# Kernel tuning notes

Hardware: AMD Instinct MI355X
Metric: run time of the kernel (lower is better)

Reference implementation:

```python
import jax, jax.numpy as jnp
import numpy as np

COMMIT_LAMBDA = 0.25


def setup_inputs() -> dict:
    key = jax.random.key(0)
    k1, k2 = jax.random.split(key)
    B, C, T = 8, 256, 1024
    NCB, K, D = 2, 8192, 128
    x = jax.random.normal(k1, (B, C, T), dtype=jnp.float32)
    # EMA codebook weights buffer (init: randn * 0.1)
    codebooks = jax.random.normal(k2, (NCB, K, D), dtype=jnp.float32) * 0.1
    return {"x": x, "codebooks": codebooks}


def reference(x, codebooks):
    B, C, T = x.shape
    ncb, K, d = codebooks.shape
    # [B, C, T] -> [B*T, ncb, d]
    xs = x.reshape(B, ncb, d, T).transpose(0, 3, 1, 2).reshape(B * T, ncb, d)
    # squared euclidean distances (argmin-equivalent to cdist)
    x2 = jnp.sum(xs * xs, axis=-1)[..., None]            # [N, ncb, 1]
    c2 = jnp.sum(codebooks * codebooks, axis=-1)[None]    # [1, ncb, K]
    xc = jnp.einsum('bnd,nkd->bnk', xs, codebooks)        # [N, ncb, K]
    d2 = x2 - 2.0 * xc + c2
    idx = jnp.argmin(d2, axis=-1)                         # [N, ncb] int
    # gather nearest code vectors: [N, ncb, d]
    q = codebooks[jnp.arange(ncb)[None, :], idx]
    # straight-through estimator
    q_st = xs + jax.lax.stop_gradient(q - xs)
    # commitment loss (training mode): sum over codebooks of mse(x_i, q_i.detach())
    loss = COMMIT_LAMBDA * jnp.sum(
        jnp.mean((xs - jax.lax.stop_gradient(q)) ** 2, axis=(0, 2))
    )
    # reassemble to [B, C, T]
    quantized = q_st.reshape(B, T, ncb, d).transpose(0, 2, 3, 1).reshape(B, C, T)
    indices = idx.reshape(B, T, ncb).transpose(0, 2, 1)   # [B, ncb, T]
    return quantized, indices, loss
```

## Files before the change

kernel.cpp:

```cpp
#include <hip/hip_runtime.h>
#include <hip/hip_bf16.h>

#define BB   8
#define TT   1024
#define NCBN 2
#define DD   128
#define KK   8192
#define MM   8192

constexpr int OUT_IDX_OFF  = BB * 256 * TT;
constexpr int OUT_LOSS_OFF = OUT_IDX_OFF + BB * NCBN * TT;

#define THR   0.45f
#define QCAP  512
#define NSPL  8

typedef __attribute__((ext_vector_type(8))) short   short8;
typedef __attribute__((ext_vector_type(4))) float   float4v;

__device__ __forceinline__ unsigned short f2bf(float v) {
    unsigned u = __float_as_uint(v);
    return (unsigned short)((u + 0x7FFFu + ((u >> 16) & 1u)) >> 16);
}

__device__ __forceinline__ void gl_lds16(const void* g, void* l) {
    __builtin_amdgcn_global_load_lds(
        (const __attribute__((address_space(1))) unsigned int*)g,
        (__attribute__((address_space(3))) unsigned int*)l, 16, 0, 0);
}

__device__ __forceinline__ unsigned fmono(float v) {
    unsigned u = __float_as_uint(v);
    return (u & 0x80000000u) ? ~u : (u | 0x80000000u);
}
__device__ __forceinline__ float fmono_inv(unsigned mu) {
    unsigned u = (mu & 0x80000000u) ? (mu & 0x7FFFFFFFu) : ~mu;
    return __uint_as_float(u);
}

__global__ __launch_bounds__(256)
void prep_kernel(const float* __restrict__ x, const float* __restrict__ cb,
                 unsigned short* __restrict__ xbf, unsigned short* __restrict__ cbf,
                 float* __restrict__ x2, float* __restrict__ c2,
                 float* __restrict__ x32t, int contig,
                 unsigned long long* __restrict__ pmin,
                 unsigned int* __restrict__ gminU,
                 float* __restrict__ out) {
    const int bx = blockIdx.x;
    const int tid = threadIdx.x;

    if (bx >= 256) {
        int g = (bx - 256) * 256 + tid;
        if (g == 0) out[OUT_LOSS_OFF] = 0.f;
        const float4* crow = (const float4*)(cb + (size_t)g * DD);
        unsigned short* orow = cbf + (size_t)g * DD;
        float s = 0.f;
#pragma unroll 4
        for (int i2 = 0; i2 < 16; ++i2) {
            float4 v0 = crow[2 * i2];
            float4 v1 = crow[2 * i2 + 1];
            s = fmaf(v0.x, v0.x, s); s = fmaf(v0.y, v0.y, s);
            s = fmaf(v0.z, v0.z, s); s = fmaf(v0.w, v0.w, s);
            s = fmaf(v1.x, v1.x, s); s = fmaf(v1.y, v1.y, s);
            s = fmaf(v1.z, v1.z, s); s = fmaf(v1.w, v1.w, s);
            uint4 pk;
            pk.x = (unsigned)f2bf(v0.x) | ((unsigned)f2bf(v0.y) << 16);
            pk.y = (unsigned)f2bf(v0.z) | ((unsigned)f2bf(v0.w) << 16);
            pk.z = (unsigned)f2bf(v1.x) | ((unsigned)f2bf(v1.y) << 16);
            pk.w = (unsigned)f2bf(v1.z) | ((unsigned)f2bf(v1.w) << 16);
            *(uint4*)(orow + i2 * 8) = pk;
        }
        c2[g] = s;
        return;
    }

    __shared__ float Ld[DD][65];
    const int b = bx >> 5, n = (bx >> 4) & 1;
    const int t0 = (bx & 15) * 64;

    const float* base = x + ((size_t)(b * 256 + n * 128)) * TT + t0;
    const int dro = tid >> 2, q4 = tid & 3;
#pragma unroll
    for (int half = 0; half < 2; ++half) {
        int d = dro + half * 64;
        const float* rp = base + (size_t)d * TT + q4 * 16;
#pragma unroll
        for (int j = 0; j < 4; ++j) {
            float4 v = *(const float4*)(rp + j * 4);
            int t = q4 * 16 + j * 4;
            Ld[d][t + 0] = v.x; Ld[d][t + 1] = v.y;
            Ld[d][t + 2] = v.z; Ld[d][t + 3] = v.w;
        }
    }
    __syncthreads();

    if (tid < 64) {
        float s = 0.f;
        for (int d = 0; d < DD; ++d) { float v = Ld[d][tid]; s = fmaf(v, v, s); }
        size_t gi = (size_t)n * MM + b * TT + t0 + tid;
        x2[gi] = s;
        pmin[gi] = 0xFFFFFFFFFFFFFFFFull;
        gminU[gi] = 0xFFFFFFFFu;
    }

    unsigned short* orow0 = xbf + ((size_t)n * MM + b * TT + t0) * DD;
#pragma unroll
    for (int pp = 0; pp < 4; ++pp) {
        int u = tid + pp * 256;
        int tt = u >> 4, sg = u & 15;
        unsigned short tmp[8];
#pragma unroll
        for (int j = 0; j < 8; ++j) tmp[j] = f2bf(Ld[sg * 8 + j][tt]);
        uint4 pk;
        pk.x = (unsigned)tmp[0] | ((unsigned)tmp[1] << 16);
        pk.y = (unsigned)tmp[2] | ((unsigned)tmp[3] << 16);
        pk.z = (unsigned)tmp[4] | ((unsigned)tmp[5] << 16);
        pk.w = (unsigned)tmp[6] | ((unsigned)tmp[7] << 16);
        *(uint4*)(orow0 + (size_t)tt * DD + sg * 8) = pk;
    }

    if (contig) {
        float* xrow0 = x32t + ((size_t)n * MM + b * TT + t0) * DD;
#pragma unroll
        for (int pp = 0; pp < 8; ++pp) {
            int u = tid + pp * 256;
            int tt = u >> 5, sg = u & 31;
            float4 v = { Ld[sg * 4 + 0][tt], Ld[sg * 4 + 1][tt],
                         Ld[sg * 4 + 2][tt], Ld[sg * 4 + 3][tt] };
            *(float4*)(xrow0 + (size_t)tt * DD + sg * 4) = v;
        }
    }
}

__device__ void rescore_one(int n, int m, int k,
                            const float* __restrict__ xex, int contig,
                            const float* __restrict__ cb,
                            const float* __restrict__ x2, const float* __restrict__ c2,
                            unsigned long long* __restrict__ pmin) {
    const float* xp; int st;
    if (contig) { xp = xex + ((size_t)n * MM + m) * DD; st = 1; }
    else {
        int b = m >> 10, t = m & (TT - 1);
        xp = xex + ((size_t)(b * 256 + n * 128)) * TT + t; st = TT;
    }
    const float* cp = cb + ((size_t)(n * KK + k)) * DD;
    float xc = 0.f;
    for (int d = 0; d < DD; ++d)
        xc = fmaf(xp[(size_t)d * st], cp[d], xc);
    float u = x2[(size_t)n * MM + m] - 2.0f * xc;
    float s = u + c2[n * KK + k];
    unsigned long long pk = ((unsigned long long)__float_as_uint(s) << 32) | (unsigned)k;
    atomicMin(pmin + (size_t)n * MM + m, pk);
}

__global__ __launch_bounds__(256, 2)
void screen_kernel(const unsigned short* __restrict__ xbf,
                   const unsigned short* __restrict__ cbf,
                   const float* __restrict__ c2,
                   const float* __restrict__ xex, int contig,
                   const float* __restrict__ cb32,
                   const float* __restrict__ x2,
                   unsigned int* __restrict__ gminU,
                   unsigned long long* __restrict__ pmin) {
    __shared__ __align__(16) unsigned short Bsh[128 * 128];
    __shared__ unsigned int       minU[128];
    __shared__ float              c2s[128];
    __shared__ unsigned int       qcnt;
    __shared__ unsigned long long queue[QCAP];

    const int tid = threadIdx.x;
    const int id  = blockIdx.x;
    const int n   = id & 1;
    const int ks  = (id >> 1) & 7;
    const int qt  = id >> 4;
    const int m0  = qt * 128;
    const int k0  = ks * 1024;

    const int wave = tid >> 6, lane = tid & 63;
    const int cw = wave & 1, qw = wave >> 1;
    const int quad = lane >> 4, l15 = lane & 15;

    int goff[8];
#pragma unroll
    for (int p = 0; p < 8; ++p) {
        int u   = (p * 4 + wave) * 64 + lane;
        int row = u >> 4;
        int seg = (u & 15) ^ (row & 15);
        goff[p] = (row * DD + seg * 8) * 2;
    }

    {
        const char* src = (const char*)(xbf + ((size_t)n * MM + m0) * DD);
#pragma unroll
        for (int p = 0; p < 8; ++p)
            gl_lds16(src + goff[p], &Bsh[(p * 4 + wave) * 512]);
    }
    if (tid < 128) minU[tid] = 0xFFFFFFFFu;
    if (tid == 0)  qcnt = 0;
    __syncthreads();

    short8 bfr[4][4];
#pragma unroll
    for (int tq = 0; tq < 4; ++tq) {
        int q = qw * 64 + tq * 16 + l15;
#pragma unroll
        for (int k4 = 0; k4 < 4; ++k4) {
            int seg = k4 * 4 + quad;
            bfr[tq][k4] = *(const short8*)(&Bsh[q * 128 + ((seg ^ l15) * 8)]);
        }
    }

    float mloc[4] = {3.4e38f, 3.4e38f, 3.4e38f, 3.4e38f};
    float thr[4]  = {3.4e38f, 3.4e38f, 3.4e38f, 3.4e38f};

    const char*  asrc0 = (const char*)(cbf + ((size_t)n * KK + k0) * DD);
    const float* c2p   = c2 + (size_t)n * KK + k0;

#pragma unroll
    for (int phase = 0; phase < 2; ++phase) {
        for (int ch = 0; ch < 8; ++ch) {
            __syncthreads();
            {
                const char* src = asrc0 + (size_t)ch * (128 * DD * 2);
#pragma unroll
                for (int p = 0; p < 8; ++p)
                    gl_lds16(src + goff[p], &Bsh[(p * 4 + wave) * 512]);
                if (tid < 32)
                    *(float4*)&c2s[tid * 4] =
                        *(const float4*)(c2p + ch * 128 + tid * 4);
            }
            __syncthreads();

            float4v acc[4][4];
#pragma unroll
            for (int tc = 0; tc < 4; ++tc)
#pragma unroll
                for (int tq = 0; tq < 4; ++tq)
                    acc[tc][tq] = (float4v){0.f, 0.f, 0.f, 0.f};

#pragma unroll
            for (int k4 = 0; k4 < 4; ++k4) {
                short8 a[4];
#pragma unroll
                for (int tc = 0; tc < 4; ++tc) {
                    int r = cw * 64 + tc * 16 + l15;
                    int seg = k4 * 4 + quad;
                    a[tc] = *(const short8*)(&Bsh[r * 128 + ((seg ^ l15) * 8)]);
                }
#pragma unroll
                for (int tc = 0; tc < 4; ++tc)
#pragma unroll
                    for (int tq = 0; tq < 4; ++tq)
                        acc[tc][tq] = __builtin_amdgcn_mfma_f32_16x16x32_bf16(
                            a[tc], bfr[tq][k4], acc[tc][tq], 0, 0, 0);
            }

#pragma unroll
            for (int tc = 0; tc < 4; ++tc) {
                float4v c2r = *(const float4v*)(&c2s[cw * 64 + tc * 16 + quad * 4]);
#pragma unroll
                for (int tq = 0; tq < 4; ++tq) {
                    float y0 = fmaf(-2.0f, acc[tc][tq][0], c2r[0]);
                    float y1 = fmaf(-2.0f, acc[tc][tq][1], c2r[1]);
                    float y2 = fmaf(-2.0f, acc[tc][tq][2], c2r[2]);
                    float y3 = fmaf(-2.0f, acc[tc][tq][3], c2r[3]);
                    float m4 = fminf(fminf(y0, y1), fminf(y2, y3));
                    if (phase == 0) {
                        mloc[tq] = fminf(mloc[tq], m4);
                    } else if (m4 <= thr[tq]) {
                        float yv[4] = {y0, y1, y2, y3};
#pragma unroll
                        for (int rg = 0; rg < 4; ++rg) {
                            if (yv[rg] <= thr[tq]) {
                                unsigned idx  = atomicAdd(&qcnt, 1u);
                                unsigned code = (unsigned)(ch * 128 + cw * 64 + tc * 16 + quad * 4 + rg);
                                unsigned q    = (unsigned)(qw * 64 + tq * 16 + l15);
                                if (idx < QCAP)
                                    queue[idx] = ((unsigned long long)__float_as_uint(yv[rg]) << 32)
                                               | (q << 10) | code;
                                else rescore_one(n, m0 + (int)q, k0 + (int)code,
                                                 xex, contig, cb32, x2, c2, pmin);
                            }
                        }
                    }
                }
            }
        }

        if (phase == 0) {
#pragma unroll
            for (int tq = 0; tq < 4; ++tq) {
                float v = mloc[tq];
                v = fminf(v, __shfl_xor(v, 16, 64));
                v = fminf(v, __shfl_xor(v, 32, 64));
                if (quad == 0)
                    atomicMin(&minU[qw * 64 + tq * 16 + l15], fmono(v));
            }
            __syncthreads();
            if (tid < 128)
                atomicMin(&gminU[(size_t)n * MM + m0 + tid], minU[tid]);
#pragma unroll
            for (int tq = 0; tq < 4; ++tq)
                thr[tq] = fmono_inv(minU[qw * 64 + tq * 16 + l15]) + THR;
        }
    }

    __syncthreads();
    if (tid < 128) {
        unsigned mu = atomicMin(&gminU[(size_t)n * MM + m0 + tid], 0xFFFFFFFFu);
        c2s[tid] = fmono_inv(mu) + THR;
    }
    __syncthreads();

    unsigned total = qcnt; if (total > QCAP) total = QCAP;
    for (unsigned i = tid; i < total; i += 256) {
        unsigned long long e = queue[i];
        float y = __uint_as_float((unsigned)(e >> 32));
        unsigned q = ((unsigned)e >> 10) & 127u;
        unsigned code = (unsigned)e & 1023u;
        if (y <= c2s[q])
            rescore_one(n, m0 + (int)q, k0 + (int)code,
                        xex, contig, cb32, x2, c2, pmin);
    }
}

__global__ __launch_bounds__(256)
void gather_kernel(const float* __restrict__ x, const float* __restrict__ cb,
                   const unsigned long long* __restrict__ pmin,
                   float* __restrict__ out) {
    __shared__ float Cr[64][DD + 1];
    __shared__ int   kid[64];
    const int b = blockIdx.x >> 1, n = blockIdx.x & 1;
    const int t0 = blockIdx.y * 64;
    const int tid = threadIdx.x;

    if (tid < 64) {
        int t = t0 + tid;
        int k = (int)(pmin[(size_t)n * MM + b * TT + t] & 0xFFFFFFFFull);
        kid[tid] = k;
        out[OUT_IDX_OFF + (b * NCBN + n) * TT + t] = (float)k;
    }
    __syncthreads();

    {
        int row = tid >> 2, q4 = tid & 3;
        const float* cp = cb + ((size_t)n * KK + kid[row]) * DD + q4 * 32;
#pragma unroll
        for (int j = 0; j < 8; ++j) {
            float4 v = *(const float4*)(cp + j * 4);
            int d = q4 * 32 + j * 4;
            Cr[row][d + 0] = v.x; Cr[row][d + 1] = v.y;
            Cr[row][d + 2] = v.z; Cr[row][d + 3] = v.w;
        }
    }
    __syncthreads();

    float lsum = 0.f;
    const float* xb = x  + ((size_t)(b * 256 + n * 128)) * TT + t0;
    float*       ob = out + ((size_t)(b * 256 + n * 128)) * TT + t0;
#pragma unroll
    for (int pp = 0; pp < 8; ++pp) {
        int u  = tid + pp * 256;
        int d  = u >> 4, ts = (u & 15) * 4;
        float4 xv = *(const float4*)(xb + (size_t)d * TT + ts);
        float4 qv = { Cr[ts + 0][d], Cr[ts + 1][d], Cr[ts + 2][d], Cr[ts + 3][d] };
        *(float4*)(ob + (size_t)d * TT + ts) = qv;
        float e;
        e = xv.x - qv.x; lsum = fmaf(e, e, lsum);
        e = xv.y - qv.y; lsum = fmaf(e, e, lsum);
        e = xv.z - qv.z; lsum = fmaf(e, e, lsum);
        e = xv.w - qv.w; lsum = fmaf(e, e, lsum);
    }

#pragma unroll
    for (int o = 32; o > 0; o >>= 1) lsum += __shfl_down(lsum, o, 64);
    __shared__ float wsum[4];
    int lane = tid & 63, w = tid >> 6;
    if (lane == 0) wsum[w] = lsum;
    __syncthreads();
    if (tid == 0) {
        float tot = wsum[0] + wsum[1] + wsum[2] + wsum[3];
        atomicAdd(out + OUT_LOSS_OFF, tot * 2.384185791015625e-7f);
    }
}

extern "C" void kernel_launch(void* const* d_in, const int* in_sizes, int n_in,
                              void* d_out, int out_size, void* d_ws, size_t ws_size,
                              hipStream_t stream) {
    (void)in_sizes; (void)n_in; (void)out_size;
    const float* x  = (const float*)d_in[0];
    const float* cb = (const float*)d_in[1];
    float* out = (float*)d_out;

    char* ws = (char*)d_ws;
    unsigned short* xbf = (unsigned short*)(ws);
    unsigned short* cbf = (unsigned short*)(ws + (4u << 20));
    float* x2 = (float*)(ws + (8u << 20));
    float* c2 = (float*)(ws + (8u << 20) + (64u << 10));
    unsigned long long* pmin =
        (unsigned long long*)(ws + (8u << 20) + (128u << 10));
    unsigned int* gminU =
        (unsigned int*)(ws + (8u << 20) + (256u << 10));
    float* x32t = (float*)(ws + (9u << 20));

    const size_t need = (9u << 20) + (size_t)NCBN * MM * DD * 4;
    const int contig = (ws_size >= need) ? 1 : 0;
    const float* xex = contig ? x32t : x;

    prep_kernel<<<dim3(320), 256, 0, stream>>>(x, cb, xbf, cbf, x2, c2,
                                               x32t, contig, pmin, gminU, out);
    screen_kernel<<<dim3(1024), 256, 0, stream>>>(xbf, cbf, c2, xex, contig,
                                                  cb, x2, gminU, pmin);
    gather_kernel<<<dim3(16, 16), 256, 0, stream>>>(x, cb, pmin, out);
}
```

Baseline: 196.7 us.

## Single-pass screening with direct-register loads and fused last-block gather

The screen kernel drops the two-phase LDS-staged MFMA loop. It loads codebook and query bf16 fragments straight from global memory into registers with double buffering, and tightens a running threshold in one pass, seeded from a shared global minimum and refreshed mid-way. The gather kernel is folded into the screen kernel: the last split-block for each query tile, found through an atomic counter, writes indices, quantized output and loss. The queue capacity is raised so fewer candidates overflow to immediate rescoring. This removes a kernel launch, the LDS traffic and the phase-0 pass over codes. The cost is uncoalesced global fragment loads, per-thread strided gather stores, and thresholds that now depend on the order blocks run in.

```diff
diff --git a/kernel.cpp b/kernel.cpp
--- a/kernel.cpp
+++ b/kernel.cpp
@@ -12,7 +12,7 @@
 constexpr int OUT_LOSS_OFF = OUT_IDX_OFF + BB * NCBN * TT;
 
 #define THR   0.45f
-#define QCAP  512
+#define QCAP  6144
 #define NSPL  8
 
 typedef __attribute__((ext_vector_type(8))) short   short8;
@@ -22,13 +22,6 @@
     unsigned u = __float_as_uint(v);
     return (unsigned short)((u + 0x7FFFu + ((u >> 16) & 1u)) >> 16);
 }
-
-__device__ __forceinline__ void gl_lds16(const void* g, void* l) {
-    __builtin_amdgcn_global_load_lds(
-        (const __attribute__((address_space(1))) unsigned int*)g,
-        (__attribute__((address_space(3))) unsigned int*)l, 16, 0, 0);
-}
-
 __device__ __forceinline__ unsigned fmono(float v) {
     unsigned u = __float_as_uint(v);
     return (u & 0x80000000u) ? ~u : (u | 0x80000000u);
@@ -45,6 +38,7 @@
                  float* __restrict__ x32t, int contig,
                  unsigned long long* __restrict__ pmin,
                  unsigned int* __restrict__ gminU,
+                 unsigned int* __restrict__ gcnt,
                  float* __restrict__ out) {
     const int bx = blockIdx.x;
     const int tid = threadIdx.x;
@@ -52,6 +46,7 @@
     if (bx >= 256) {
         int g = (bx - 256) * 256 + tid;
         if (g == 0) out[OUT_LOSS_OFF] = 0.f;
+        if (bx == 256 && tid < 128) gcnt[tid] = 0u;
         const float4* crow = (const float4*)(cb + (size_t)g * DD);
         unsigned short* orow = cbf + (size_t)g * DD;
         float s = 0.f;
@@ -100,7 +95,7 @@
         size_t gi = (size_t)n * MM + b * TT + t0 + tid;
         x2[gi] = s;
         pmin[gi] = 0xFFFFFFFFFFFFFFFFull;
-        gminU[gi] = 0xFFFFFFFFu;
+        gminU[gi] = fmono(3.4e38f);
     }
 
     unsigned short* orow0 = xbf + ((size_t)n * MM + b * TT + t0) * DD;
@@ -161,12 +156,15 @@
                    const float* __restrict__ cb32,
                    const float* __restrict__ x2,
                    unsigned int* __restrict__ gminU,
-                   unsigned long long* __restrict__ pmin) {
-    __shared__ __align__(16) unsigned short Bsh[128 * 128];
-    __shared__ unsigned int       minU[128];
-    __shared__ float              c2s[128];
-    __shared__ unsigned int       qcnt;
+                   unsigned long long* __restrict__ pmin,
+                   unsigned int* __restrict__ gcnt,
+                   float* __restrict__ out) {
     __shared__ unsigned long long queue[QCAP];
+    __shared__ unsigned int qcnt;
+    __shared__ float gthr[128];
+    __shared__ int   kid[128];
+    __shared__ float wred[4];
+    __shared__ int   dflag;
 
     const int tid = threadIdx.x;
     const int id  = blockIdx.x;
@@ -180,56 +178,41 @@
     const int cw = wave & 1, qw = wave >> 1;
     const int quad = lane >> 4, l15 = lane & 15;
 
-    int goff[8];
-#pragma unroll
-    for (int p = 0; p < 8; ++p) {
-        int u   = (p * 4 + wave) * 64 + lane;
-        int row = u >> 4;
-        int seg = (u & 15) ^ (row & 15);
-        goff[p] = (row * DD + seg * 8) * 2;
-    }
-
-    {
-        const char* src = (const char*)(xbf + ((size_t)n * MM + m0) * DD);
-#pragma unroll
-        for (int p = 0; p < 8; ++p)
-            gl_lds16(src + goff[p], &Bsh[(p * 4 + wave) * 512]);
-    }
-    if (tid < 128) minU[tid] = 0xFFFFFFFFu;
-    if (tid == 0)  qcnt = 0;
-    __syncthreads();
+    if (tid == 0) qcnt = 0;
 
     short8 bfr[4][4];
-#pragma unroll
-    for (int tq = 0; tq < 4; ++tq) {
-        int q = qw * 64 + tq * 16 + l15;
-#pragma unroll
-        for (int k4 = 0; k4 < 4; ++k4) {
-            int seg = k4 * 4 + quad;
-            bfr[tq][k4] = *(const short8*)(&Bsh[q * 128 + ((seg ^ l15) * 8)]);
-        }
-    }
-
-    float mloc[4] = {3.4e38f, 3.4e38f, 3.4e38f, 3.4e38f};
-    float thr[4]  = {3.4e38f, 3.4e38f, 3.4e38f, 3.4e38f};
-
-    const char*  asrc0 = (const char*)(cbf + ((size_t)n * KK + k0) * DD);
-    const float* c2p   = c2 + (size_t)n * KK + k0;
-
-#pragma unroll
-    for (int phase = 0; phase < 2; ++phase) {
-        for (int ch = 0; ch < 8; ++ch) {
-            __syncthreads();
-            {
-                const char* src = asrc0 + (size_t)ch * (128 * DD * 2);
-#pragma unroll
-                for (int p = 0; p < 8; ++p)
-                    gl_lds16(src + goff[p], &Bsh[(p * 4 + wave) * 512]);
-                if (tid < 32)
-                    *(float4*)&c2s[tid * 4] =
-                        *(const float4*)(c2p + ch * 128 + tid * 4);
-            }
-            __syncthreads();
+    const unsigned short* Qb = xbf + ((size_t)(n * MM + m0 + qw * 64 + l15)) * DD + quad * 8;
+#pragma unroll
+    for (int tq = 0; tq < 4; ++tq)
+#pragma unroll
+        for (int k4 = 0; k4 < 4; ++k4)
+            bfr[tq][k4] = *(const short8*)(Qb + tq * 16 * DD + k4 * 32);
+
+    const size_t gq = (size_t)n * MM + m0;
+    float mloc[4];
+#pragma unroll
+    for (int tq = 0; tq < 4; ++tq)
+        mloc[tq] = fmono_inv(gminU[gq + qw * 64 + tq * 16 + l15]);
+    const int startpass = (fmono_inv(gminU[gq]) > 1.0e37f) ? 0 : 1;
+
+    __syncthreads();
+
+    const unsigned short* Ab = cbf + ((size_t)(n * KK + k0 + cw * 64 + l15)) * DD + quad * 8;
+    const float* C2b = c2 + (size_t)n * KK + k0 + cw * 64 + quad * 4;
+
+    for (int pass = startpass; pass < 2; ++pass) {
+        const int nch = (pass == 0) ? 1 : 8;
+        const unsigned short* Abch = Ab;
+        short8 abuf[2][4];
+#pragma unroll
+        for (int tc = 0; tc < 4; ++tc)
+            abuf[0][tc] = *(const short8*)(Abch + tc * 16 * DD);
+
+        for (int ch = 0; ch < nch; ++ch) {
+            float4 c2r4[4];
+#pragma unroll
+            for (int tc = 0; tc < 4; ++tc)
+                c2r4[tc] = *(const float4*)(C2b + ch * 128 + tc * 16);
 
             float4v acc[4][4];
 #pragma unroll
@@ -240,44 +223,44 @@
 
 #pragma unroll
             for (int k4 = 0; k4 < 4; ++k4) {
-                short8 a[4];
-#pragma unroll
-                for (int tc = 0; tc < 4; ++tc) {
-                    int r = cw * 64 + tc * 16 + l15;
-                    int seg = k4 * 4 + quad;
-                    a[tc] = *(const short8*)(&Bsh[r * 128 + ((seg ^ l15) * 8)]);
-                }
+                const unsigned short* pb =
+                    (k4 < 3) ? (Abch + (k4 + 1) * 32)
+                             : ((ch + 1 < nch) ? (Abch + 128 * DD) : Ab);
+#pragma unroll
+                for (int tc = 0; tc < 4; ++tc)
+                    abuf[(k4 + 1) & 1][tc] = *(const short8*)(pb + tc * 16 * DD);
 #pragma unroll
                 for (int tc = 0; tc < 4; ++tc)
 #pragma unroll
                     for (int tq = 0; tq < 4; ++tq)
                         acc[tc][tq] = __builtin_amdgcn_mfma_f32_16x16x32_bf16(
-                            a[tc], bfr[tq][k4], acc[tc][tq], 0, 0, 0);
+                            abuf[k4 & 1][tc], bfr[tq][k4], acc[tc][tq], 0, 0, 0);
             }
 
 #pragma unroll
             for (int tc = 0; tc < 4; ++tc) {
-                float4v c2r = *(const float4v*)(&c2s[cw * 64 + tc * 16 + quad * 4]);
 #pragma unroll
                 for (int tq = 0; tq < 4; ++tq) {
-                    float y0 = fmaf(-2.0f, acc[tc][tq][0], c2r[0]);
-                    float y1 = fmaf(-2.0f, acc[tc][tq][1], c2r[1]);
-                    float y2 = fmaf(-2.0f, acc[tc][tq][2], c2r[2]);
-                    float y3 = fmaf(-2.0f, acc[tc][tq][3], c2r[3]);
+                    float y0 = fmaf(-2.0f, acc[tc][tq][0], c2r4[tc].x);
+                    float y1 = fmaf(-2.0f, acc[tc][tq][1], c2r4[tc].y);
+                    float y2 = fmaf(-2.0f, acc[tc][tq][2], c2r4[tc].z);
+                    float y3 = fmaf(-2.0f, acc[tc][tq][3], c2r4[tc].w);
                     float m4 = fminf(fminf(y0, y1), fminf(y2, y3));
-                    if (phase == 0) {
-                        mloc[tq] = fminf(mloc[tq], m4);
-                    } else if (m4 <= thr[tq]) {
+                    bool gate = (m4 <= mloc[tq] + THR);
+                    mloc[tq] = fminf(mloc[tq], m4);
+                    if (pass == 1 && gate) {
                         float yv[4] = {y0, y1, y2, y3};
+                        float th = mloc[tq] + THR;
 #pragma unroll
                         for (int rg = 0; rg < 4; ++rg) {
-                            if (yv[rg] <= thr[tq]) {
+                            if (yv[rg] <= th) {
                                 unsigned idx  = atomicAdd(&qcnt, 1u);
                                 unsigned code = (unsigned)(ch * 128 + cw * 64 + tc * 16 + quad * 4 + rg);
                                 unsigned q    = (unsigned)(qw * 64 + tq * 16 + l15);
-                                if (idx < QCAP)
-                                    queue[idx] = ((unsigned long long)__float_as_uint(yv[rg]) << 32)
-                                               | (q << 10) | code;
+                                unsigned long long ent =
+                                    ((unsigned long long)__float_as_uint(yv[rg]) << 32)
+                                    | (q << 10) | code;
+                                if (idx < QCAP) queue[idx] = ent;
                                 else rescore_one(n, m0 + (int)q, k0 + (int)code,
                                                  xex, contig, cb32, x2, c2, pmin);
                             }
@@ -285,31 +268,33 @@
                     }
                 }
             }
-        }
-
-        if (phase == 0) {
+
 #pragma unroll
             for (int tq = 0; tq < 4; ++tq) {
                 float v = mloc[tq];
                 v = fminf(v, __shfl_xor(v, 16, 64));
                 v = fminf(v, __shfl_xor(v, 32, 64));
                 if (quad == 0)
-                    atomicMin(&minU[qw * 64 + tq * 16 + l15], fmono(v));
+                    atomicMin(&gminU[gq + qw * 64 + tq * 16 + l15], fmono(v));
             }
-            __syncthreads();
-            if (tid < 128)
-                atomicMin(&gminU[(size_t)n * MM + m0 + tid], minU[tid]);
+            if (pass == 1 && ch == 3) {
+#pragma unroll
+                for (int tq = 0; tq < 4; ++tq)
+                    mloc[tq] = fminf(mloc[tq],
+                        fmono_inv(gminU[gq + qw * 64 + tq * 16 + l15]));
+            }
+            Abch += 128 * DD;
+        }
+        if (pass == 0) {
 #pragma unroll
             for (int tq = 0; tq < 4; ++tq)
-                thr[tq] = fmono_inv(minU[qw * 64 + tq * 16 + l15]) + THR;
-        }
-    }
-
-    __syncthreads();
-    if (tid < 128) {
-        unsigned mu = atomicMin(&gminU[(size_t)n * MM + m0 + tid], 0xFFFFFFFFu);
-        c2s[tid] = fmono_inv(mu) + THR;
-    }
+                mloc[tq] = fminf(mloc[tq],
+                    fmono_inv(gminU[gq + qw * 64 + tq * 16 + l15]));
+        }
+    }
+
+    __syncthreads();
+    if (tid < 128) gthr[tid] = fmono_inv(gminU[gq + tid]) + THR;
     __syncthreads();
 
     unsigned total = qcnt; if (total > QCAP) total = QCAP;
@@ -318,68 +303,52 @@
         float y = __uint_as_float((unsigned)(e >> 32));
         unsigned q = ((unsigned)e >> 10) & 127u;
         unsigned code = (unsigned)e & 1023u;
-        if (y <= c2s[q])
+        if (y <= gthr[q])
             rescore_one(n, m0 + (int)q, k0 + (int)code,
                         xex, contig, cb32, x2, c2, pmin);
     }
-}
-
-__global__ __launch_bounds__(256)
-void gather_kernel(const float* __restrict__ x, const float* __restrict__ cb,
-                   const unsigned long long* __restrict__ pmin,
-                   float* __restrict__ out) {
-    __shared__ float Cr[64][DD + 1];
-    __shared__ int   kid[64];
-    const int b = blockIdx.x >> 1, n = blockIdx.x & 1;
-    const int t0 = blockIdx.y * 64;
-    const int tid = threadIdx.x;
-
-    if (tid < 64) {
-        int t = t0 + tid;
-        int k = (int)(pmin[(size_t)n * MM + b * TT + t] & 0xFFFFFFFFull);
+
+    __threadfence();
+    __syncthreads();
+    if (tid == 0)
+        dflag = (atomicAdd(&gcnt[(n << 6) | qt], 1u) == NSPL - 1) ? 1 : 0;
+    __syncthreads();
+    if (!dflag) return;
+    __threadfence();
+
+    const int b = qt >> 3;
+    const int t0g = (qt & 7) * 128;
+    if (tid < 128) {
+        unsigned long long e = atomicMin(&pmin[gq + tid], 0xFFFFFFFFFFFFFFFFull);
+        int k = (int)(e & 0xFFFFFFFFull);
         kid[tid] = k;
-        out[OUT_IDX_OFF + (b * NCBN + n) * TT + t] = (float)k;
-    }
-    __syncthreads();
-
-    {
-        int row = tid >> 2, q4 = tid & 3;
-        const float* cp = cb + ((size_t)n * KK + kid[row]) * DD + q4 * 32;
-#pragma unroll
-        for (int j = 0; j < 8; ++j) {
-            float4 v = *(const float4*)(cp + j * 4);
-            int d = q4 * 32 + j * 4;
-            Cr[row][d + 0] = v.x; Cr[row][d + 1] = v.y;
-            Cr[row][d + 2] = v.z; Cr[row][d + 3] = v.w;
-        }
-    }
-    __syncthreads();
+        out[OUT_IDX_OFF + (b * NCBN + n) * TT + t0g + tid] = (float)k;
+    }
+    __syncthreads();
+
+    const int q = tid & 127, hf = tid >> 7;
+    const int k = kid[q];
+    const float* cp = cb32 + ((size_t)n * KK + k) * DD + hf * 64;
+    const float* xp; int st;
+    if (contig) { xp = xex + ((size_t)n * MM + m0 + q) * DD + hf * 64; st = 1; }
+    else        { xp = xex + ((size_t)(b * 256 + n * 128 + hf * 64)) * TT + t0g + q; st = TT; }
+    float* ob = out + ((size_t)(b * 256 + n * 128 + hf * 64)) * TT + t0g + q;
 
     float lsum = 0.f;
-    const float* xb = x  + ((size_t)(b * 256 + n * 128)) * TT + t0;
-    float*       ob = out + ((size_t)(b * 256 + n * 128)) * TT + t0;
-#pragma unroll
-    for (int pp = 0; pp < 8; ++pp) {
-        int u  = tid + pp * 256;
-        int d  = u >> 4, ts = (u & 15) * 4;
-        float4 xv = *(const float4*)(xb + (size_t)d * TT + ts);
-        float4 qv = { Cr[ts + 0][d], Cr[ts + 1][d], Cr[ts + 2][d], Cr[ts + 3][d] };
-        *(float4*)(ob + (size_t)d * TT + ts) = qv;
-        float e;
-        e = xv.x - qv.x; lsum = fmaf(e, e, lsum);
-        e = xv.y - qv.y; lsum = fmaf(e, e, lsum);
-        e = xv.z - qv.z; lsum = fmaf(e, e, lsum);
-        e = xv.w - qv.w; lsum = fmaf(e, e, lsum);
+#pragma unroll 4
+    for (int j = 0; j < 64; ++j) {
+        float qv = cp[j];
+        float xv = xp[(size_t)j * st];
+        ob[(size_t)j * TT] = qv;
+        float e = xv - qv; lsum = fmaf(e, e, lsum);
     }
 
 #pragma unroll
     for (int o = 32; o > 0; o >>= 1) lsum += __shfl_down(lsum, o, 64);
-    __shared__ float wsum[4];
-    int lane = tid & 63, w = tid >> 6;
-    if (lane == 0) wsum[w] = lsum;
+    if (lane == 0) wred[wave] = lsum;
     __syncthreads();
     if (tid == 0) {
-        float tot = wsum[0] + wsum[1] + wsum[2] + wsum[3];
+        float tot = wred[0] + wred[1] + wred[2] + wred[3];
         atomicAdd(out + OUT_LOSS_OFF, tot * 2.384185791015625e-7f);
     }
 }
@@ -401,6 +370,8 @@
         (unsigned long long*)(ws + (8u << 20) + (128u << 10));
     unsigned int* gminU =
         (unsigned int*)(ws + (8u << 20) + (256u << 10));
+    unsigned int* gcnt =
+        (unsigned int*)(ws + (8u << 20) + (320u << 10));
     float* x32t = (float*)(ws + (9u << 20));
 
     const size_t need = (9u << 20) + (size_t)NCBN * MM * DD * 4;
@@ -408,8 +379,7 @@
     const float* xex = contig ? x32t : x;
 
     prep_kernel<<<dim3(320), 256, 0, stream>>>(x, cb, xbf, cbf, x2, c2,
-                                               x32t, contig, pmin, gminU, out);
+                                               x32t, contig, pmin, gminU, gcnt, out);
     screen_kernel<<<dim3(1024), 256, 0, stream>>>(xbf, cbf, c2, xex, contig,
-                                                  cb, x2, gminU, pmin);
-    gather_kernel<<<dim3(16, 16), 256, 0, stream>>>(x, cb, pmin, out);
-}
+                                                  cb, x2, gminU, pmin, gcnt, out);
+}
```

Result: slower. 349.7 us (+77.7%).
